# Kernel optimization log

Hardware: AMD Instinct MI355X
Metric: run time of the kernel (lower is better)

The kernel has to match this reference:

```python
import jax, jax.numpy as jnp
import numpy as np

E = 384      # n_embed
H = 6        # n_head
HS = E // H  # head_size = 64
B = 64
T = 256      # == block_size
FF = 4 * E


def _layernorm(x, g, b, eps=1e-5):
    m = x.mean(-1, keepdims=True)
    v = ((x - m) ** 2).mean(-1, keepdims=True)
    return (x - m) / jnp.sqrt(v + eps) * g + b


def _mha(q_in, k_in, v_in, wq, bq, wk, bk, wv, bv, pw, pb):
    # Faithful to source: scale uses q_in's last dim (n_embed=384), NOT head_size,
    # and the causal tril mask is applied even in cross-attention.
    scale = q_in.shape[-1] ** -0.5
    q = jnp.einsum('bte,hes->bhts', q_in, wq) + bq[None, :, None, :]  # [B,H,T1,HS]
    k = jnp.einsum('bue,hes->bhus', k_in, wk) + bk[None, :, None, :]  # [B,H,T2,HS]
    v = jnp.einsum('bue,hes->bhus', v_in, wv) + bv[None, :, None, :]
    wei = jnp.einsum('bhts,bhus->bhtu', q, k) * scale                 # [B,H,T1,T2]
    T1, T2 = q_in.shape[1], k_in.shape[1]
    mask = jnp.tril(jnp.ones((T1, T2), dtype=bool))
    wei = jnp.where(mask[None, None], wei, -jnp.inf)
    wei = jax.nn.softmax(wei, axis=-1)
    out = jnp.einsum('bhtu,bhus->bths', wei, v)                       # [B,T1,H,HS]
    out = out.reshape(out.shape[0], out.shape[1], -1)                 # concat heads
    return out @ pw + pb


def setup_inputs() -> dict:
    key = jax.random.key(0)
    ks = jax.random.split(key, 32)
    s = 0.02
    d = {
        'encode_output': jax.random.normal(ks[0], (B, T, E), jnp.float32),
        'x': jax.random.normal(ks[1], (B, T, E), jnp.float32),
    }
    i = 2
    for p in ('sa1', 'sa2'):
        d[p + '_wq'] = jax.random.normal(ks[i], (H, E, HS), jnp.float32) * s; i += 1
        d[p + '_bq'] = jnp.zeros((H, HS), jnp.float32)
        d[p + '_wk'] = jax.random.normal(ks[i], (H, E, HS), jnp.float32) * s; i += 1
        d[p + '_bk'] = jnp.zeros((H, HS), jnp.float32)
        d[p + '_wv'] = jax.random.normal(ks[i], (H, E, HS), jnp.float32) * s; i += 1
        d[p + '_bv'] = jnp.zeros((H, HS), jnp.float32)
        d[p + '_pw'] = jax.random.normal(ks[i], (E, E), jnp.float32) * s; i += 1
        d[p + '_pb'] = jnp.zeros((E,), jnp.float32)
    d['ff_w1'] = jax.random.normal(ks[i], (E, FF), jnp.float32) * s; i += 1
    d['ff_b1'] = jnp.zeros((FF,), jnp.float32)
    d['ff_w2'] = jax.random.normal(ks[i], (FF, E), jnp.float32) * s; i += 1
    d['ff_b2'] = jnp.zeros((E,), jnp.float32)
    for n in ('ln1', 'ln2', 'ln3'):
        d[n + '_g'] = jnp.ones((E,), jnp.float32)
        d[n + '_b'] = jnp.zeros((E,), jnp.float32)
    return d


def reference(encode_output, x,
              sa1_wq, sa1_bq, sa1_wk, sa1_bk, sa1_wv, sa1_bv, sa1_pw, sa1_pb,
              sa2_wq, sa2_bq, sa2_wk, sa2_bk, sa2_wv, sa2_bv, sa2_pw, sa2_pb,
              ff_w1, ff_b1, ff_w2, ff_b2,
              ln1_g, ln1_b, ln2_g, ln2_b, ln3_g, ln3_b):
    # masked self-attention + add&norm
    a1 = _mha(x, x, x, sa1_wq, sa1_bq, sa1_wk, sa1_bk, sa1_wv, sa1_bv, sa1_pw, sa1_pb)
    o1 = _layernorm(x + a1, ln1_g, ln1_b)
    # cross-attention (q=o1, k=v=encode_output) + add&norm
    a2 = _mha(o1, encode_output, encode_output,
              sa2_wq, sa2_bq, sa2_wk, sa2_bk, sa2_wv, sa2_bv, sa2_pw, sa2_pb)
    o2 = _layernorm(o1 + a2, ln2_g, ln2_b)
    # FFN + add&norm
    f = jax.nn.relu(o2 @ ff_w1 + ff_b1) @ ff_w2 + ff_b2
    return _layernorm(o2 + f, ln3_g, ln3_b)
```

## Files before the change

kernel.cpp:

```cpp
#include <hip/hip_runtime.h>

typedef __attribute__((ext_vector_type(8))) short bf16x8;
typedef __attribute__((ext_vector_type(4))) float f32x4;

__device__ __forceinline__ float b2f(ushort b) {
    union { unsigned int u; float f; } x;
    x.u = ((unsigned int)b) << 16;
    return x.f;
}
__device__ __forceinline__ ushort f2b(float f) {
    union { float f; unsigned int u; } x;
    x.f = f;
    unsigned int r = x.u + 0x7fffu + ((x.u >> 16) & 1u);
    return (ushort)(r >> 16);
}
__device__ __forceinline__ int4 pack8(float4 a, float4 b) {
    union { int4 v; ushort u[8]; } r;
    r.u[0] = f2b(a.x); r.u[1] = f2b(a.y); r.u[2] = f2b(a.z); r.u[3] = f2b(a.w);
    r.u[4] = f2b(b.x); r.u[5] = f2b(b.y); r.u[6] = f2b(b.z); r.u[7] = f2b(b.w);
    return r.v;
}
__device__ __forceinline__ void gl2lds16(const ushort* g, ushort* l) {
    __builtin_amdgcn_global_load_lds(
        (const __attribute__((address_space(1))) void*)g,
        (__attribute__((address_space(3))) void*)l, 16, 0, 0);
}

__global__ __launch_bounds__(256) void gemm_bt(
    const ushort* __restrict__ A, const ushort* __restrict__ Bt,
    ushort* __restrict__ C, const float* __restrict__ bias,
    const ushort* __restrict__ resb, const float* __restrict__ resf,
    int M, int N, int K, int relu)
{
    __shared__ __align__(16) ushort As[2][128 * 32];
    __shared__ __align__(16) ushort Bs[2][128 * 32];
    const int tid  = threadIdx.x;
    const int wave = tid >> 6, lane = tid & 63;
    const int wm = wave >> 1, wn = wave & 1;
    const int qd = lane >> 4, lc = lane & 15;
    const int row0 = blockIdx.y * 128, col0 = blockIdx.x * 128;
    const int sr = lane >> 2;
    const int sc = (lane & 3) * 8;

    const ushort* Ag  = A  + (size_t)(row0 + wave * 32 + sr) * K + sc;
    const ushort* Ag2 = Ag + (size_t)16 * K;
    const ushort* Bg  = Bt + (size_t)(col0 + wave * 32 + sr) * K + sc;
    const ushort* Bg2 = Bg + (size_t)16 * K;

    f32x4 acc[4][4];
#pragma unroll
    for (int i = 0; i < 4; i++)
#pragma unroll
        for (int j = 0; j < 4; j++) acc[i][j] = 0.0f;

    for (int k0 = 0; k0 < K; k0 += 64) {
        gl2lds16(Ag  + k0,      &As[0][wave * 1024]);
        gl2lds16(Ag2 + k0,      &As[0][wave * 1024 + 512]);
        gl2lds16(Bg  + k0,      &Bs[0][wave * 1024]);
        gl2lds16(Bg2 + k0,      &Bs[0][wave * 1024 + 512]);
        gl2lds16(Ag  + k0 + 32, &As[1][wave * 1024]);
        gl2lds16(Ag2 + k0 + 32, &As[1][wave * 1024 + 512]);
        gl2lds16(Bg  + k0 + 32, &Bs[1][wave * 1024]);
        gl2lds16(Bg2 + k0 + 32, &Bs[1][wave * 1024 + 512]);
        __syncthreads();

#pragma unroll
        for (int c = 0; c < 2; c++) {
            bf16x8 af[4], bfr[4];
#pragma unroll
            for (int mi = 0; mi < 4; mi++)
                af[mi] = *(const bf16x8*)&As[c][(wm * 64 + mi * 16 + lc) * 32 + qd * 8];
#pragma unroll
            for (int ni = 0; ni < 4; ni++)
                bfr[ni] = *(const bf16x8*)&Bs[c][(wn * 64 + ni * 16 + lc) * 32 + qd * 8];
#pragma unroll
            for (int mi = 0; mi < 4; mi++)
#pragma unroll
                for (int ni = 0; ni < 4; ni++)
                    acc[mi][ni] = __builtin_amdgcn_mfma_f32_16x16x32_bf16(
                        af[mi], bfr[ni], acc[mi][ni], 0, 0, 0);
        }
        __syncthreads();
    }

#pragma unroll
    for (int mi = 0; mi < 4; mi++) {
#pragma unroll
        for (int r = 0; r < 4; r++) {
            int grow = row0 + wm * 64 + mi * 16 + qd * 4 + r;
#pragma unroll
            for (int ni = 0; ni < 4; ni++) {
                int gcol = col0 + wn * 64 + ni * 16 + lc;
                float v = acc[mi][ni][r];
                if (bias) v += bias[gcol];
                if (resb) v += b2f(resb[(size_t)grow * N + gcol]);
                if (resf) v += resf[(size_t)grow * N + gcol];
                if (relu) v = fmaxf(v, 0.0f);
                C[(size_t)grow * N + gcol] = f2b(v);
            }
        }
    }
}

__global__ __launch_bounds__(256) void gemm_n64(
    const ushort* __restrict__ A, const ushort* __restrict__ Bt,
    ushort* __restrict__ C, const float* __restrict__ bias,
    const ushort* __restrict__ resb, const float* __restrict__ resf,
    int M, int N, int K, int relu)
{
    __shared__ __align__(16) ushort As[2][128 * 32];
    __shared__ __align__(16) ushort Bs[2][64 * 32];
    const int tid  = threadIdx.x;
    const int wave = tid >> 6, lane = tid & 63;
    const int qd = lane >> 4, lc = lane & 15;
    const int row0 = blockIdx.y * 128, col0 = blockIdx.x * 64;
    const int sr = lane >> 2;
    const int sc = (lane & 3) * 8;

    const ushort* Ag  = A  + (size_t)(row0 + wave * 32 + sr) * K + sc;
    const ushort* Ag2 = Ag + (size_t)16 * K;
    const ushort* Bg  = Bt + (size_t)(col0 + wave * 16 + sr) * K + sc;

    f32x4 acc[2][4];
#pragma unroll
    for (int i = 0; i < 2; i++)
#pragma unroll
        for (int j = 0; j < 4; j++) acc[i][j] = 0.0f;

    for (int k0 = 0; k0 < K; k0 += 64) {
        gl2lds16(Ag  + k0,      &As[0][wave * 1024]);
        gl2lds16(Ag2 + k0,      &As[0][wave * 1024 + 512]);
        gl2lds16(Bg  + k0,      &Bs[0][wave * 512]);
        gl2lds16(Ag  + k0 + 32, &As[1][wave * 1024]);
        gl2lds16(Ag2 + k0 + 32, &As[1][wave * 1024 + 512]);
        gl2lds16(Bg  + k0 + 32, &Bs[1][wave * 512]);
        __syncthreads();

#pragma unroll
        for (int c = 0; c < 2; c++) {
            bf16x8 af[2], bfr[4];
#pragma unroll
            for (int mi = 0; mi < 2; mi++)
                af[mi] = *(const bf16x8*)&As[c][(wave * 32 + mi * 16 + lc) * 32 + qd * 8];
#pragma unroll
            for (int ni = 0; ni < 4; ni++)
                bfr[ni] = *(const bf16x8*)&Bs[c][(ni * 16 + lc) * 32 + qd * 8];
#pragma unroll
            for (int mi = 0; mi < 2; mi++)
#pragma unroll
                for (int ni = 0; ni < 4; ni++)
                    acc[mi][ni] = __builtin_amdgcn_mfma_f32_16x16x32_bf16(
                        af[mi], bfr[ni], acc[mi][ni], 0, 0, 0);
        }
        __syncthreads();
    }

#pragma unroll
    for (int mi = 0; mi < 2; mi++) {
#pragma unroll
        for (int r = 0; r < 4; r++) {
            int grow = row0 + wave * 32 + mi * 16 + qd * 4 + r;
#pragma unroll
            for (int ni = 0; ni < 4; ni++) {
                int gcol = col0 + ni * 16 + lc;
                float v = acc[mi][ni][r];
                if (bias) v += bias[gcol];
                if (resb) v += b2f(resb[(size_t)grow * N + gcol]);
                if (resf) v += resf[(size_t)grow * N + gcol];
                if (relu) v = fmaxf(v, 0.0f);
                C[(size_t)grow * N + gcol] = f2b(v);
            }
        }
    }
}

__global__ __launch_bounds__(256) void gemm_dual(
    const ushort* __restrict__ A1, const ushort* __restrict__ B1t,
    ushort* __restrict__ C1, const float* __restrict__ bias1, int N1,
    const ushort* __restrict__ A2, const ushort* __restrict__ B2t,
    ushort* __restrict__ C2, const float* __restrict__ bias2, int N2,
    int split, int K)
{
    __shared__ __align__(16) ushort As[2][128 * 32];
    __shared__ __align__(16) ushort Bs[2][64 * 32];
    const int tid  = threadIdx.x;
    const int wave = tid >> 6, lane = tid & 63;
    const int qd = lane >> 4, lc = lane & 15;
    const bool first = (int)blockIdx.x < split;
    const ushort* A  = first ? A1 : A2;
    const ushort* Bt = first ? B1t : B2t;
    ushort* C        = first ? C1 : C2;
    const float* bias = first ? bias1 : bias2;
    const int N      = first ? N1 : N2;
    const int col0   = (first ? blockIdx.x : blockIdx.x - split) * 64;
    const int row0   = blockIdx.y * 128;
    const int sr = lane >> 2;
    const int sc = (lane & 3) * 8;

    const ushort* Ag  = A  + (size_t)(row0 + wave * 32 + sr) * K + sc;
    const ushort* Ag2 = Ag + (size_t)16 * K;
    const ushort* Bg  = Bt + (size_t)(col0 + wave * 16 + sr) * K + sc;

    f32x4 acc[2][4];
#pragma unroll
    for (int i = 0; i < 2; i++)
#pragma unroll
        for (int j = 0; j < 4; j++) acc[i][j] = 0.0f;

    for (int k0 = 0; k0 < K; k0 += 64) {
        gl2lds16(Ag  + k0,      &As[0][wave * 1024]);
        gl2lds16(Ag2 + k0,      &As[0][wave * 1024 + 512]);
        gl2lds16(Bg  + k0,      &Bs[0][wave * 512]);
        gl2lds16(Ag  + k0 + 32, &As[1][wave * 1024]);
        gl2lds16(Ag2 + k0 + 32, &As[1][wave * 1024 + 512]);
        gl2lds16(Bg  + k0 + 32, &Bs[1][wave * 512]);
        __syncthreads();

#pragma unroll
        for (int c = 0; c < 2; c++) {
            bf16x8 af[2], bfr[4];
#pragma unroll
            for (int mi = 0; mi < 2; mi++)
                af[mi] = *(const bf16x8*)&As[c][(wave * 32 + mi * 16 + lc) * 32 + qd * 8];
#pragma unroll
            for (int ni = 0; ni < 4; ni++)
                bfr[ni] = *(const bf16x8*)&Bs[c][(ni * 16 + lc) * 32 + qd * 8];
#pragma unroll
            for (int mi = 0; mi < 2; mi++)
#pragma unroll
                for (int ni = 0; ni < 4; ni++)
                    acc[mi][ni] = __builtin_amdgcn_mfma_f32_16x16x32_bf16(
                        af[mi], bfr[ni], acc[mi][ni], 0, 0, 0);
        }
        __syncthreads();
    }

#pragma unroll
    for (int mi = 0; mi < 2; mi++) {
#pragma unroll
        for (int r = 0; r < 4; r++) {
            int grow = row0 + wave * 32 + mi * 16 + qd * 4 + r;
#pragma unroll
            for (int ni = 0; ni < 4; ni++) {
                int gcol = col0 + ni * 16 + lc;
                float v = acc[mi][ni][r] + bias[gcol];
                C[(size_t)grow * N + gcol] = f2b(v);
            }
        }
    }
}

__global__ __launch_bounds__(256) void attn(
    const ushort* __restrict__ q, int qstr,
    const ushort* __restrict__ k, int kstr,
    const ushort* __restrict__ v, int vstr,
    ushort* __restrict__ out)
{
    __shared__ __align__(16) ushort Qs[64 * 72];
    __shared__ __align__(16) ushort Kc[64 * 72];
    __shared__ __align__(16) ushort Vc[64 * 72];
    __shared__ __align__(16) ushort Ps[64 * 264];

    const int tid = threadIdx.x;
    const int wave = tid >> 6, lane = tid & 63;
    const int qd = lane >> 4, lc = lane & 15;
    const int b = blockIdx.z, h = blockIdx.y, t0 = blockIdx.x * 64;
    const int hc = h * 64;
    const float scale = 0.051031036307982884f;

    {
        int r = tid >> 2, c = (tid & 3) * 16;
        int4 q0 = *(const int4*)&q[(size_t)(b * 256 + t0 + r) * qstr + hc + c];
        int4 q1 = *(const int4*)&q[(size_t)(b * 256 + t0 + r) * qstr + hc + c + 8];
        *(int4*)&Qs[r * 72 + c] = q0;
        *(int4*)&Qs[r * 72 + c + 8] = q1;
    }

    f32x4 accS[16];
#pragma unroll
    for (int j = 0; j < 16; j++) accS[j] = 0.0f;

    for (int uc = 0; uc < 4; uc++) {
        int r = tid >> 2, c = (tid & 3) * 16;
        int4 k0v = *(const int4*)&k[(size_t)(b * 256 + uc * 64 + r) * kstr + hc + c];
        int4 k1v = *(const int4*)&k[(size_t)(b * 256 + uc * 64 + r) * kstr + hc + c + 8];
        __syncthreads();
        *(int4*)&Kc[r * 72 + c] = k0v;
        *(int4*)&Kc[r * 72 + c + 8] = k1v;
        __syncthreads();
#pragma unroll
        for (int s0 = 0; s0 < 64; s0 += 32) {
            bf16x8 a = *(const bf16x8*)&Qs[(wave * 16 + lc) * 72 + s0 + qd * 8];
#pragma unroll
            for (int ni = 0; ni < 4; ni++) {
                bf16x8 bb = *(const bf16x8*)&Kc[(ni * 16 + lc) * 72 + s0 + qd * 8];
                accS[uc * 4 + ni] =
                    __builtin_amdgcn_mfma_f32_16x16x32_bf16(a, bb, accS[uc * 4 + ni], 0, 0, 0);
            }
        }
    }

#pragma unroll
    for (int rr = 0; rr < 4; rr++) {
        int t = t0 + wave * 16 + qd * 4 + rr;
        float pv[16];
        float mx = -3.0e38f;
#pragma unroll
        for (int j = 0; j < 16; j++) {
            int u = (j >> 2) * 64 + (j & 3) * 16 + lc;
            float s = accS[j][rr] * scale;
            s = (u <= t) ? s : -3.0e38f;
            pv[j] = s;
            mx = fmaxf(mx, s);
        }
#pragma unroll
        for (int m = 1; m < 16; m <<= 1) mx = fmaxf(mx, __shfl_xor(mx, m, 16));
        float sum = 0.0f;
#pragma unroll
        for (int j = 0; j < 16; j++) { float p = __expf(pv[j] - mx); pv[j] = p; sum += p; }
#pragma unroll
        for (int m = 1; m < 16; m <<= 1) sum += __shfl_xor(sum, m, 16);
        float inv = 1.0f / sum;
#pragma unroll
        for (int j = 0; j < 16; j++) {
            int u = (j >> 2) * 64 + (j & 3) * 16 + lc;
            Ps[(wave * 16 + qd * 4 + rr) * 264 + u] = f2b(pv[j] * inv);
        }
    }

    f32x4 accO[4];
#pragma unroll
    for (int j = 0; j < 4; j++) accO[j] = 0.0f;
    for (int uc = 0; uc < 4; uc++) {
        int r = tid >> 2, s0 = (tid & 3) * 16;
        int4 v0 = *(const int4*)&v[(size_t)(b * 256 + uc * 64 + r) * vstr + hc + s0];
        int4 v1 = *(const int4*)&v[(size_t)(b * 256 + uc * 64 + r) * vstr + hc + s0 + 8];
        __syncthreads();
        {
            const ushort* t0p = (const ushort*)&v0;
            const ushort* t1p = (const ushort*)&v1;
#pragma unroll
            for (int j = 0; j < 8; j++) Vc[(s0 + j) * 72 + r] = t0p[j];
#pragma unroll
            for (int j = 0; j < 8; j++) Vc[(s0 + 8 + j) * 72 + r] = t1p[j];
        }
        __syncthreads();
#pragma unroll
        for (int u0 = 0; u0 < 64; u0 += 32) {
            bf16x8 a = *(const bf16x8*)&Ps[(wave * 16 + lc) * 264 + uc * 64 + u0 + qd * 8];
#pragma unroll
            for (int ni = 0; ni < 4; ni++) {
                bf16x8 bb = *(const bf16x8*)&Vc[(ni * 16 + lc) * 72 + u0 + qd * 8];
                accO[ni] = __builtin_amdgcn_mfma_f32_16x16x32_bf16(a, bb, accO[ni], 0, 0, 0);
            }
        }
    }

#pragma unroll
    for (int ni = 0; ni < 4; ni++)
#pragma unroll
        for (int rr = 0; rr < 4; rr++) {
            int t = t0 + wave * 16 + qd * 4 + rr;
            out[(size_t)(b * 256 + t) * 384 + hc + ni * 16 + lc] = f2b(accO[ni][rr]);
        }
}

__global__ __launch_bounds__(256) void lnorm(
    const ushort* __restrict__ in, const float* __restrict__ g,
    const float* __restrict__ be, ushort* __restrict__ outb,
    float* __restrict__ outf)
{
    const int wave = threadIdx.x >> 6, lane = threadIdx.x & 63;
    const int row = blockIdx.x * 4 + wave;
    const ushort* r = in + (size_t)row * 384;
    float x[6], s1 = 0.0f, s2 = 0.0f;
#pragma unroll
    for (int j = 0; j < 6; j++) {
        x[j] = b2f(r[j * 64 + lane]);
        s1 += x[j]; s2 += x[j] * x[j];
    }
#pragma unroll
    for (int m = 1; m < 64; m <<= 1) {
        s1 += __shfl_xor(s1, m, 64);
        s2 += __shfl_xor(s2, m, 64);
    }
    float mean = s1 * (1.0f / 384.0f);
    float var  = s2 * (1.0f / 384.0f) - mean * mean;
    float rstd = rsqrtf(var + 1e-5f);
#pragma unroll
    for (int j = 0; j < 6; j++) {
        float y = (x[j] - mean) * rstd * g[j * 64 + lane] + be[j * 64 + lane];
        if (outb) outb[(size_t)row * 384 + j * 64 + lane] = f2b(y);
        if (outf) outf[(size_t)row * 384 + j * 64 + lane] = y;
    }
}

__global__ __launch_bounds__(256) void f32cvt(const float* __restrict__ in,
                                             ushort* __restrict__ out)
{
    size_t i = ((size_t)blockIdx.x * 256 + threadIdx.x) * 8;
    float4 a = *(const float4*)(in + i);
    float4 b = *(const float4*)(in + i + 4);
    *(int4*)(out + i) = pack8(a, b);
}

__global__ __launch_bounds__(256) void transp_t(
    const float* __restrict__ in, ushort* __restrict__ out, int R, int C)
{
    __shared__ float t[32][33];
    const int tx = threadIdx.x & 31, ty = threadIdx.x >> 5;
    const int c0 = blockIdx.x * 32, r0 = blockIdx.y * 32;
#pragma unroll
    for (int i = 0; i < 32; i += 8)
        t[ty + i][tx] = in[(size_t)(r0 + ty + i) * C + c0 + tx];
    __syncthreads();
#pragma unroll
    for (int i = 0; i < 32; i += 8)
        out[(size_t)(c0 + ty + i) * R + r0 + tx] = f2b(t[tx][ty + i]);
}

__global__ __launch_bounds__(256) void pack_qkv_t(
    const float* __restrict__ wq, const float* __restrict__ wk,
    const float* __restrict__ wv, ushort* __restrict__ Wt)
{
    __shared__ float t[32][33];
    const int tx = threadIdx.x & 31, ty = threadIdx.x >> 5;
    const int e0 = blockIdx.x * 32, s0 = blockIdx.y * 32;
    const int z = blockIdx.z, seg = z / 6, h = z - seg * 6;
    const float* w = (seg == 0) ? wq : (seg == 1) ? wk : wv;
    const float* wh = w + (size_t)h * 384 * 64;
#pragma unroll
    for (int i = 0; i < 32; i += 8)
        t[ty + i][tx] = wh[(size_t)(e0 + ty + i) * 64 + s0 + tx];
    __syncthreads();
    const int nbase = seg * 384 + h * 64 + s0;
#pragma unroll
    for (int i = 0; i < 32; i += 8)
        Wt[(size_t)(nbase + ty + i) * 384 + e0 + tx] = f2b(t[tx][ty + i]);
}

__global__ __launch_bounds__(256) void biaspack(
    const float* __restrict__ q1, const float* __restrict__ k1, const float* __restrict__ v1,
    const float* __restrict__ q2, const float* __restrict__ k2, const float* __restrict__ v2,
    float* __restrict__ b1, float* __restrict__ b2)
{
    int i = blockIdx.x * 256 + threadIdx.x;
    if (i >= 2304) return;
    int grp = i / 1152, r = i - grp * 1152;
    int seg = r / 384, nn = r - seg * 384;
    const float* src = grp == 0 ? (seg == 0 ? q1 : seg == 1 ? k1 : v1)
                                : (seg == 0 ? q2 : seg == 1 ? k2 : v2);
    (grp == 0 ? b1 : b2)[r] = src[nn];
}

extern "C" void kernel_launch(void* const* d_in, const int* in_sizes, int n_in,
                              void* d_out, int out_size, void* d_ws, size_t ws_size,
                              hipStream_t stream)
{
    const float* enc = (const float*)d_in[0];
    const float* x   = (const float*)d_in[1];
    const float* s1wq = (const float*)d_in[2];  const float* s1bq = (const float*)d_in[3];
    const float* s1wk = (const float*)d_in[4];  const float* s1bk = (const float*)d_in[5];
    const float* s1wv = (const float*)d_in[6];  const float* s1bv = (const float*)d_in[7];
    const float* s1pw = (const float*)d_in[8];  const float* s1pb = (const float*)d_in[9];
    const float* s2wq = (const float*)d_in[10]; const float* s2bq = (const float*)d_in[11];
    const float* s2wk = (const float*)d_in[12]; const float* s2bk = (const float*)d_in[13];
    const float* s2wv = (const float*)d_in[14]; const float* s2bv = (const float*)d_in[15];
    const float* s2pw = (const float*)d_in[16]; const float* s2pb = (const float*)d_in[17];
    const float* fw1 = (const float*)d_in[18];  const float* fb1 = (const float*)d_in[19];
    const float* fw2 = (const float*)d_in[20];  const float* fb2 = (const float*)d_in[21];
    const float* g1 = (const float*)d_in[22];   const float* be1 = (const float*)d_in[23];
    const float* g2 = (const float*)d_in[24];   const float* be2 = (const float*)d_in[25];
    const float* g3 = (const float*)d_in[26];   const float* be3 = (const float*)d_in[27];

    if (ws_size < 80216064u) return;

    ushort* wsp = (ushort*)d_ws;
    ushort* qkv1 = wsp;
    ushort* q2   = wsp;
    ushort* kv2  = wsp + 6291456;
    ushort* h1   = wsp;
    ushort* att  = wsp + 18874368;
    ushort* xb   = wsp + 18874368;
    ushort* tmp  = wsp + 25165824;
    ushort* o1b  = wsp + 31457280;
    ushort* W1   = wsp + 37748736;
    ushort* W2   = W1 + 442368;
    ushort* pw1t = W2 + 442368;
    ushort* pw2t = pw1t + 147456;
    ushort* w1t  = pw2t + 147456;
    ushort* w2t  = w1t + 589824;

    ushort* encb = (ushort*)d_out;
    ushort* o2b  = (ushort*)d_out;
    float* bias1 = (float*)((ushort*)d_out + 6291456);
    float* bias2 = bias1 + 1152;

    f32cvt<<<dim3(3072), dim3(256), 0, stream>>>(x, xb);
    f32cvt<<<dim3(3072), dim3(256), 0, stream>>>(enc, encb);
    pack_qkv_t<<<dim3(12, 2, 18), dim3(256), 0, stream>>>(s1wq, s1wk, s1wv, W1);
    pack_qkv_t<<<dim3(12, 2, 18), dim3(256), 0, stream>>>(s2wq, s2wk, s2wv, W2);
    biaspack<<<dim3(9), dim3(256), 0, stream>>>(s1bq, s1bk, s1bv, s2bq, s2bk, s2bv, bias1, bias2);
    transp_t<<<dim3(12, 12), dim3(256), 0, stream>>>(s1pw, pw1t, 384, 384);
    transp_t<<<dim3(12, 12), dim3(256), 0, stream>>>(s2pw, pw2t, 384, 384);
    transp_t<<<dim3(48, 12), dim3(256), 0, stream>>>(fw1, w1t, 384, 1536);
    transp_t<<<dim3(12, 48), dim3(256), 0, stream>>>(fw2, w2t, 1536, 384);

    gemm_bt<<<dim3(9, 128), dim3(256), 0, stream>>>(xb, W1, qkv1, bias1, nullptr, nullptr, 16384, 1152, 384, 0);
    attn<<<dim3(4, 6, 64), dim3(256), 0, stream>>>(qkv1, 1152, qkv1 + 384, 1152, qkv1 + 768, 1152, att);
    gemm_n64<<<dim3(6, 128), dim3(256), 0, stream>>>(att, pw1t, tmp, s1pb, nullptr, x, 16384, 384, 384, 0);
    lnorm<<<dim3(4096), dim3(256), 0, stream>>>(tmp, g1, be1, o1b, nullptr);

    gemm_dual<<<dim3(18, 128), dim3(256), 0, stream>>>(
        o1b, W2, q2, bias2, 384,
        encb, W2 + 147456, kv2, bias2 + 384, 768, 6, 384);
    attn<<<dim3(4, 6, 64), dim3(256), 0, stream>>>(q2, 384, kv2, 768, kv2 + 384, 768, att);
    gemm_n64<<<dim3(6, 128), dim3(256), 0, stream>>>(att, pw2t, tmp, s2pb, o1b, nullptr, 16384, 384, 384, 0);
    lnorm<<<dim3(4096), dim3(256), 0, stream>>>(tmp, g2, be2, o2b, nullptr);

    gemm_bt<<<dim3(12, 128), dim3(256), 0, stream>>>(o2b, w1t, h1, fb1, nullptr, nullptr, 16384, 1536, 384, 1);
    gemm_n64<<<dim3(6, 128), dim3(256), 0, stream>>>(h1, w2t, tmp, fb2, o2b, nullptr, 16384, 384, 1536, 0);
    lnorm<<<dim3(4096), dim3(256), 0, stream>>>(tmp, g3, be3, nullptr, (float*)d_out);
}
```

Before: 537.6 us.

## Register-prefetch GEMM staging and merge prep kernels into one launch

The three GEMM kernels stop using direct global-to-LDS loads of two 32-wide K chunks per barrier pair. They now stage a single 32-wide chunk through registers: the next chunk's global loads are issued before the MFMA work on the current chunk, which halves LDS use. Separately, the nine small conversion, transpose and bias-pack launches are fused into one prep_all kernel that dispatches on block index, cutting launch overhead. The cost is twice as many barriers per unit of K and extra VGPRs for the prefetch registers.

```diff
diff --git a/kernel.cpp b/kernel.cpp
--- a/kernel.cpp
+++ b/kernel.cpp
@@ -20,11 +20,6 @@
     r.u[4] = f2b(b.x); r.u[5] = f2b(b.y); r.u[6] = f2b(b.z); r.u[7] = f2b(b.w);
     return r.v;
 }
-__device__ __forceinline__ void gl2lds16(const ushort* g, ushort* l) {
-    __builtin_amdgcn_global_load_lds(
-        (const __attribute__((address_space(1))) void*)g,
-        (__attribute__((address_space(3))) void*)l, 16, 0, 0);
-}
 
 __global__ __launch_bounds__(256) void gemm_bt(
     const ushort* __restrict__ A, const ushort* __restrict__ Bt,
@@ -32,20 +27,20 @@
     const ushort* __restrict__ resb, const float* __restrict__ resf,
     int M, int N, int K, int relu)
 {
-    __shared__ __align__(16) ushort As[2][128 * 32];
-    __shared__ __align__(16) ushort Bs[2][128 * 32];
+    __shared__ __align__(16) ushort As[128 * 32];
+    __shared__ __align__(16) ushort Bs[128 * 32];
     const int tid  = threadIdx.x;
     const int wave = tid >> 6, lane = tid & 63;
     const int wm = wave >> 1, wn = wave & 1;
     const int qd = lane >> 4, lc = lane & 15;
     const int row0 = blockIdx.y * 128, col0 = blockIdx.x * 128;
-    const int sr = lane >> 2;
-    const int sc = (lane & 3) * 8;
-
-    const ushort* Ag  = A  + (size_t)(row0 + wave * 32 + sr) * K + sc;
-    const ushort* Ag2 = Ag + (size_t)16 * K;
-    const ushort* Bg  = Bt + (size_t)(col0 + wave * 32 + sr) * K + sc;
-    const ushort* Bg2 = Bg + (size_t)16 * K;
+
+    const int srow = tid >> 1;
+    const int scol = (tid & 1) * 16;
+    const ushort* Ag = A  + (size_t)(row0 + srow) * K + scol;
+    const ushort* Bg = Bt + (size_t)(col0 + srow) * K + scol;
+    ushort* Asd = &As[srow * 32 + scol];
+    ushort* Bsd = &Bs[srow * 32 + scol];
 
     f32x4 acc[4][4];
 #pragma unroll
@@ -53,34 +48,36 @@
 #pragma unroll
         for (int j = 0; j < 4; j++) acc[i][j] = 0.0f;
 
-    for (int k0 = 0; k0 < K; k0 += 64) {
-        gl2lds16(Ag  + k0,      &As[0][wave * 1024]);
-        gl2lds16(Ag2 + k0,      &As[0][wave * 1024 + 512]);
-        gl2lds16(Bg  + k0,      &Bs[0][wave * 1024]);
-        gl2lds16(Bg2 + k0,      &Bs[0][wave * 1024 + 512]);
-        gl2lds16(Ag  + k0 + 32, &As[1][wave * 1024]);
-        gl2lds16(Ag2 + k0 + 32, &As[1][wave * 1024 + 512]);
-        gl2lds16(Bg  + k0 + 32, &Bs[1][wave * 1024]);
-        gl2lds16(Bg2 + k0 + 32, &Bs[1][wave * 1024 + 512]);
-        __syncthreads();
-
-#pragma unroll
-        for (int c = 0; c < 2; c++) {
-            bf16x8 af[4], bfr[4];
-#pragma unroll
-            for (int mi = 0; mi < 4; mi++)
-                af[mi] = *(const bf16x8*)&As[c][(wm * 64 + mi * 16 + lc) * 32 + qd * 8];
+    int4 a0 = *(const int4*)(Ag);
+    int4 a1 = *(const int4*)(Ag + 8);
+    int4 b0 = *(const int4*)(Bg);
+    int4 b1 = *(const int4*)(Bg + 8);
+
+    for (int k0 = 0; k0 < K; k0 += 32) {
+        __syncthreads();
+        *(int4*)Asd = a0; *(int4*)(Asd + 8) = a1;
+        *(int4*)Bsd = b0; *(int4*)(Bsd + 8) = b1;
+        if (k0 + 32 < K) {
+            a0 = *(const int4*)(Ag + k0 + 32);
+            a1 = *(const int4*)(Ag + k0 + 40);
+            b0 = *(const int4*)(Bg + k0 + 32);
+            b1 = *(const int4*)(Bg + k0 + 40);
+        }
+        __syncthreads();
+
+        bf16x8 af[4], bfr[4];
+#pragma unroll
+        for (int mi = 0; mi < 4; mi++)
+            af[mi] = *(const bf16x8*)&As[(wm * 64 + mi * 16 + lc) * 32 + qd * 8];
+#pragma unroll
+        for (int ni = 0; ni < 4; ni++)
+            bfr[ni] = *(const bf16x8*)&Bs[(wn * 64 + ni * 16 + lc) * 32 + qd * 8];
+#pragma unroll
+        for (int mi = 0; mi < 4; mi++)
 #pragma unroll
             for (int ni = 0; ni < 4; ni++)
-                bfr[ni] = *(const bf16x8*)&Bs[c][(wn * 64 + ni * 16 + lc) * 32 + qd * 8];
-#pragma unroll
-            for (int mi = 0; mi < 4; mi++)
-#pragma unroll
-                for (int ni = 0; ni < 4; ni++)
-                    acc[mi][ni] = __builtin_amdgcn_mfma_f32_16x16x32_bf16(
-                        af[mi], bfr[ni], acc[mi][ni], 0, 0, 0);
-        }
-        __syncthreads();
+                acc[mi][ni] = __builtin_amdgcn_mfma_f32_16x16x32_bf16(
+                    af[mi], bfr[ni], acc[mi][ni], 0, 0, 0);
     }
 
 #pragma unroll
@@ -108,18 +105,21 @@
     const ushort* __restrict__ resb, const float* __restrict__ resf,
     int M, int N, int K, int relu)
 {
-    __shared__ __align__(16) ushort As[2][128 * 32];
-    __shared__ __align__(16) ushort Bs[2][64 * 32];
+    __shared__ __align__(16) ushort As[128 * 32];
+    __shared__ __align__(16) ushort Bs[64 * 32];
     const int tid  = threadIdx.x;
     const int wave = tid >> 6, lane = tid & 63;
     const int qd = lane >> 4, lc = lane & 15;
     const int row0 = blockIdx.y * 128, col0 = blockIdx.x * 64;
-    const int sr = lane >> 2;
-    const int sc = (lane & 3) * 8;
-
-    const ushort* Ag  = A  + (size_t)(row0 + wave * 32 + sr) * K + sc;
-    const ushort* Ag2 = Ag + (size_t)16 * K;
-    const ushort* Bg  = Bt + (size_t)(col0 + wave * 16 + sr) * K + sc;
+
+    const int srow = tid >> 1;
+    const int scol = (tid & 1) * 16;
+    const ushort* Ag = A + (size_t)(row0 + srow) * K + scol;
+    ushort* Asd = &As[srow * 32 + scol];
+    const int brow = tid >> 2;
+    const int bcol = (tid & 3) * 8;
+    const ushort* Bg = Bt + (size_t)(col0 + brow) * K + bcol;
+    ushort* Bsd = &Bs[brow * 32 + bcol];
 
     f32x4 acc[2][4];
 #pragma unroll
@@ -127,32 +127,34 @@
 #pragma unroll
         for (int j = 0; j < 4; j++) acc[i][j] = 0.0f;
 
-    for (int k0 = 0; k0 < K; k0 += 64) {
-        gl2lds16(Ag  + k0,      &As[0][wave * 1024]);
-        gl2lds16(Ag2 + k0,      &As[0][wave * 1024 + 512]);
-        gl2lds16(Bg  + k0,      &Bs[0][wave * 512]);
-        gl2lds16(Ag  + k0 + 32, &As[1][wave * 1024]);
-        gl2lds16(Ag2 + k0 + 32, &As[1][wave * 1024 + 512]);
-        gl2lds16(Bg  + k0 + 32, &Bs[1][wave * 512]);
-        __syncthreads();
-
-#pragma unroll
-        for (int c = 0; c < 2; c++) {
-            bf16x8 af[2], bfr[4];
-#pragma unroll
-            for (int mi = 0; mi < 2; mi++)
-                af[mi] = *(const bf16x8*)&As[c][(wave * 32 + mi * 16 + lc) * 32 + qd * 8];
+    int4 a0 = *(const int4*)(Ag);
+    int4 a1 = *(const int4*)(Ag + 8);
+    int4 b0 = *(const int4*)(Bg);
+
+    for (int k0 = 0; k0 < K; k0 += 32) {
+        __syncthreads();
+        *(int4*)Asd = a0; *(int4*)(Asd + 8) = a1;
+        *(int4*)Bsd = b0;
+        if (k0 + 32 < K) {
+            a0 = *(const int4*)(Ag + k0 + 32);
+            a1 = *(const int4*)(Ag + k0 + 40);
+            b0 = *(const int4*)(Bg + k0 + 32);
+        }
+        __syncthreads();
+
+        bf16x8 af[2], bfr[4];
+#pragma unroll
+        for (int mi = 0; mi < 2; mi++)
+            af[mi] = *(const bf16x8*)&As[(wave * 32 + mi * 16 + lc) * 32 + qd * 8];
+#pragma unroll
+        for (int ni = 0; ni < 4; ni++)
+            bfr[ni] = *(const bf16x8*)&Bs[(ni * 16 + lc) * 32 + qd * 8];
+#pragma unroll
+        for (int mi = 0; mi < 2; mi++)
 #pragma unroll
             for (int ni = 0; ni < 4; ni++)
-                bfr[ni] = *(const bf16x8*)&Bs[c][(ni * 16 + lc) * 32 + qd * 8];
-#pragma unroll
-            for (int mi = 0; mi < 2; mi++)
-#pragma unroll
-                for (int ni = 0; ni < 4; ni++)
-                    acc[mi][ni] = __builtin_amdgcn_mfma_f32_16x16x32_bf16(
-                        af[mi], bfr[ni], acc[mi][ni], 0, 0, 0);
-        }
-        __syncthreads();
+                acc[mi][ni] = __builtin_amdgcn_mfma_f32_16x16x32_bf16(
+                    af[mi], bfr[ni], acc[mi][ni], 0, 0, 0);
     }
 
 #pragma unroll
@@ -181,8 +183,8 @@
     ushort* __restrict__ C2, const float* __restrict__ bias2, int N2,
     int split, int K)
 {
-    __shared__ __align__(16) ushort As[2][128 * 32];
-    __shared__ __align__(16) ushort Bs[2][64 * 32];
+    __shared__ __align__(16) ushort As[128 * 32];
+    __shared__ __align__(16) ushort Bs[64 * 32];
     const int tid  = threadIdx.x;
     const int wave = tid >> 6, lane = tid & 63;
     const int qd = lane >> 4, lc = lane & 15;
@@ -194,12 +196,15 @@
     const int N      = first ? N1 : N2;
     const int col0   = (first ? blockIdx.x : blockIdx.x - split) * 64;
     const int row0   = blockIdx.y * 128;
-    const int sr = lane >> 2;
-    const int sc = (lane & 3) * 8;
-
-    const ushort* Ag  = A  + (size_t)(row0 + wave * 32 + sr) * K + sc;
-    const ushort* Ag2 = Ag + (size_t)16 * K;
-    const ushort* Bg  = Bt + (size_t)(col0 + wave * 16 + sr) * K + sc;
+
+    const int srow = tid >> 1;
+    const int scol = (tid & 1) * 16;
+    const ushort* Ag = A + (size_t)(row0 + srow) * K + scol;
+    ushort* Asd = &As[srow * 32 + scol];
+    const int brow = tid >> 2;
+    const int bcol = (tid & 3) * 8;
+    const ushort* Bg = Bt + (size_t)(col0 + brow) * K + bcol;
+    ushort* Bsd = &Bs[brow * 32 + bcol];
 
     f32x4 acc[2][4];
 #pragma unroll
@@ -207,32 +212,34 @@
 #pragma unroll
         for (int j = 0; j < 4; j++) acc[i][j] = 0.0f;
 
-    for (int k0 = 0; k0 < K; k0 += 64) {
-        gl2lds16(Ag  + k0,      &As[0][wave * 1024]);
-        gl2lds16(Ag2 + k0,      &As[0][wave * 1024 + 512]);
-        gl2lds16(Bg  + k0,      &Bs[0][wave * 512]);
-        gl2lds16(Ag  + k0 + 32, &As[1][wave * 1024]);
-        gl2lds16(Ag2 + k0 + 32, &As[1][wave * 1024 + 512]);
-        gl2lds16(Bg  + k0 + 32, &Bs[1][wave * 512]);
-        __syncthreads();
-
-#pragma unroll
-        for (int c = 0; c < 2; c++) {
-            bf16x8 af[2], bfr[4];
-#pragma unroll
-            for (int mi = 0; mi < 2; mi++)
-                af[mi] = *(const bf16x8*)&As[c][(wave * 32 + mi * 16 + lc) * 32 + qd * 8];
+    int4 a0 = *(const int4*)(Ag);
+    int4 a1 = *(const int4*)(Ag + 8);
+    int4 b0 = *(const int4*)(Bg);
+
+    for (int k0 = 0; k0 < K; k0 += 32) {
+        __syncthreads();
+        *(int4*)Asd = a0; *(int4*)(Asd + 8) = a1;
+        *(int4*)Bsd = b0;
+        if (k0 + 32 < K) {
+            a0 = *(const int4*)(Ag + k0 + 32);
+            a1 = *(const int4*)(Ag + k0 + 40);
+            b0 = *(const int4*)(Bg + k0 + 32);
+        }
+        __syncthreads();
+
+        bf16x8 af[2], bfr[4];
+#pragma unroll
+        for (int mi = 0; mi < 2; mi++)
+            af[mi] = *(const bf16x8*)&As[(wave * 32 + mi * 16 + lc) * 32 + qd * 8];
+#pragma unroll
+        for (int ni = 0; ni < 4; ni++)
+            bfr[ni] = *(const bf16x8*)&Bs[(ni * 16 + lc) * 32 + qd * 8];
+#pragma unroll
+        for (int mi = 0; mi < 2; mi++)
 #pragma unroll
             for (int ni = 0; ni < 4; ni++)
-                bfr[ni] = *(const bf16x8*)&Bs[c][(ni * 16 + lc) * 32 + qd * 8];
-#pragma unroll
-            for (int mi = 0; mi < 2; mi++)
-#pragma unroll
-                for (int ni = 0; ni < 4; ni++)
-                    acc[mi][ni] = __builtin_amdgcn_mfma_f32_16x16x32_bf16(
-                        af[mi], bfr[ni], acc[mi][ni], 0, 0, 0);
-        }
-        __syncthreads();
+                acc[mi][ni] = __builtin_amdgcn_mfma_f32_16x16x32_bf16(
+                    af[mi], bfr[ni], acc[mi][ni], 0, 0, 0);
     }
 
 #pragma unroll
@@ -395,21 +402,17 @@
     }
 }
 
-__global__ __launch_bounds__(256) void f32cvt(const float* __restrict__ in,
-                                             ushort* __restrict__ out)
-{
-    size_t i = ((size_t)blockIdx.x * 256 + threadIdx.x) * 8;
+__device__ __forceinline__ void dev_cvt(const float* in, ushort* out, int blk) {
+    size_t i = ((size_t)blk * 256 + threadIdx.x) * 8;
     float4 a = *(const float4*)(in + i);
     float4 b = *(const float4*)(in + i + 4);
     *(int4*)(out + i) = pack8(a, b);
 }
-
-__global__ __launch_bounds__(256) void transp_t(
-    const float* __restrict__ in, ushort* __restrict__ out, int R, int C)
-{
-    __shared__ float t[32][33];
+__device__ __forceinline__ void dev_transp(const float* in, ushort* out,
+                                           int R, int C, int bx, int by,
+                                           float (*t)[33]) {
     const int tx = threadIdx.x & 31, ty = threadIdx.x >> 5;
-    const int c0 = blockIdx.x * 32, r0 = blockIdx.y * 32;
+    const int c0 = bx * 32, r0 = by * 32;
 #pragma unroll
     for (int i = 0; i < 32; i += 8)
         t[ty + i][tx] = in[(size_t)(r0 + ty + i) * C + c0 + tx];
@@ -418,15 +421,13 @@
     for (int i = 0; i < 32; i += 8)
         out[(size_t)(c0 + ty + i) * R + r0 + tx] = f2b(t[tx][ty + i]);
 }
-
-__global__ __launch_bounds__(256) void pack_qkv_t(
-    const float* __restrict__ wq, const float* __restrict__ wk,
-    const float* __restrict__ wv, ushort* __restrict__ Wt)
-{
-    __shared__ float t[32][33];
+__device__ __forceinline__ void dev_packqkv(const float* wq, const float* wk,
+                                            const float* wv, ushort* Wt,
+                                            int blk, float (*t)[33]) {
     const int tx = threadIdx.x & 31, ty = threadIdx.x >> 5;
-    const int e0 = blockIdx.x * 32, s0 = blockIdx.y * 32;
-    const int z = blockIdx.z, seg = z / 6, h = z - seg * 6;
+    const int bx = blk % 12, by = (blk / 12) % 2, bz = blk / 24;
+    const int e0 = bx * 32, s0 = by * 32;
+    const int seg = bz / 6, h = bz - seg * 6;
     const float* w = (seg == 0) ? wq : (seg == 1) ? wk : wv;
     const float* wh = w + (size_t)h * 384 * 64;
 #pragma unroll
@@ -439,18 +440,47 @@
         Wt[(size_t)(nbase + ty + i) * 384 + e0 + tx] = f2b(t[tx][ty + i]);
 }
 
-__global__ __launch_bounds__(256) void biaspack(
-    const float* __restrict__ q1, const float* __restrict__ k1, const float* __restrict__ v1,
-    const float* __restrict__ q2, const float* __restrict__ k2, const float* __restrict__ v2,
-    float* __restrict__ b1, float* __restrict__ b2)
-{
-    int i = blockIdx.x * 256 + threadIdx.x;
+__global__ __launch_bounds__(256) void prep_all(
+    const float* __restrict__ x, ushort* __restrict__ xb,
+    const float* __restrict__ enc, ushort* __restrict__ encb,
+    const float* __restrict__ s1wq, const float* __restrict__ s1wk,
+    const float* __restrict__ s1wv, ushort* __restrict__ W1,
+    const float* __restrict__ s2wq, const float* __restrict__ s2wk,
+    const float* __restrict__ s2wv, ushort* __restrict__ W2,
+    const float* __restrict__ s1pw, ushort* __restrict__ pw1t,
+    const float* __restrict__ s2pw, ushort* __restrict__ pw2t,
+    const float* __restrict__ fw1, ushort* __restrict__ w1t,
+    const float* __restrict__ fw2, ushort* __restrict__ w2t,
+    const float* __restrict__ s1bq, const float* __restrict__ s1bk,
+    const float* __restrict__ s1bv, const float* __restrict__ s2bq,
+    const float* __restrict__ s2bk, const float* __restrict__ s2bv,
+    float* __restrict__ bias1, float* __restrict__ bias2)
+{
+    __shared__ float t[32][33];
+    int blk = blockIdx.x;
+    if (blk < 3072) { dev_cvt(x, xb, blk); return; }
+    blk -= 3072;
+    if (blk < 3072) { dev_cvt(enc, encb, blk); return; }
+    blk -= 3072;
+    if (blk < 432) { dev_packqkv(s1wq, s1wk, s1wv, W1, blk, t); return; }
+    blk -= 432;
+    if (blk < 432) { dev_packqkv(s2wq, s2wk, s2wv, W2, blk, t); return; }
+    blk -= 432;
+    if (blk < 144) { dev_transp(s1pw, pw1t, 384, 384, blk % 12, blk / 12, t); return; }
+    blk -= 144;
+    if (blk < 144) { dev_transp(s2pw, pw2t, 384, 384, blk % 12, blk / 12, t); return; }
+    blk -= 144;
+    if (blk < 576) { dev_transp(fw1, w1t, 384, 1536, blk % 48, blk / 48, t); return; }
+    blk -= 576;
+    if (blk < 576) { dev_transp(fw2, w2t, 1536, 384, blk % 12, blk / 12, t); return; }
+    blk -= 576;
+    int i = blk * 256 + threadIdx.x;
     if (i >= 2304) return;
     int grp = i / 1152, r = i - grp * 1152;
     int seg = r / 384, nn = r - seg * 384;
-    const float* src = grp == 0 ? (seg == 0 ? q1 : seg == 1 ? k1 : v1)
-                                : (seg == 0 ? q2 : seg == 1 ? k2 : v2);
-    (grp == 0 ? b1 : b2)[r] = src[nn];
+    const float* src = grp == 0 ? (seg == 0 ? s1bq : seg == 1 ? s1bk : s1bv)
+                                : (seg == 0 ? s2bq : seg == 1 ? s2bk : s2bv);
+    (grp == 0 ? bias1 : bias2)[r] = src[nn];
 }
 
 extern "C" void kernel_launch(void* const* d_in, const int* in_sizes, int n_in,
@@ -496,15 +526,11 @@
     float* bias1 = (float*)((ushort*)d_out + 6291456);
     float* bias2 = bias1 + 1152;
 
-    f32cvt<<<dim3(3072), dim3(256), 0, stream>>>(x, xb);
-    f32cvt<<<dim3(3072), dim3(256), 0, stream>>>(enc, encb);
-    pack_qkv_t<<<dim3(12, 2, 18), dim3(256), 0, stream>>>(s1wq, s1wk, s1wv, W1);
-    pack_qkv_t<<<dim3(12, 2, 18), dim3(256), 0, stream>>>(s2wq, s2wk, s2wv, W2);
-    biaspack<<<dim3(9), dim3(256), 0, stream>>>(s1bq, s1bk, s1bv, s2bq, s2bk, s2bv, bias1, bias2);
-    transp_t<<<dim3(12, 12), dim3(256), 0, stream>>>(s1pw, pw1t, 384, 384);
-    transp_t<<<dim3(12, 12), dim3(256), 0, stream>>>(s2pw, pw2t, 384, 384);
-    transp_t<<<dim3(48, 12), dim3(256), 0, stream>>>(fw1, w1t, 384, 1536);
-    transp_t<<<dim3(12, 48), dim3(256), 0, stream>>>(fw2, w2t, 1536, 384);
+    prep_all<<<dim3(8457), dim3(256), 0, stream>>>(
+        x, xb, enc, encb,
+        s1wq, s1wk, s1wv, W1, s2wq, s2wk, s2wv, W2,
+        s1pw, pw1t, s2pw, pw2t, fw1, w1t, fw2, w2t,
+        s1bq, s1bk, s1bv, s2bq, s2bk, s2bv, bias1, bias2);
 
     gemm_bt<<<dim3(9, 128), dim3(256), 0, stream>>>(xb, W1, qkv1, bias1, nullptr, nullptr, 16384, 1152, 384, 0);
     attn<<<dim3(4, 6, 64), dim3(256), 0, stream>>>(qkv1, 1152, qkv1 + 384, 1152, qkv1 + 768, 1152, att);
```

After: 498.7 us. -7.2%, faster.
